# Performance work log

Measured on AMD Instinct MI355X. Metric: run time of the kernel, lower is better.

The kernel has to match this reference:

```python
import jax, jax.numpy as jnp
import numpy as np

B, T, D_IN, H, BR, D_OUT = 256, 500, 700, 200, 2, 35
V_TH = 1.0


def setup_inputs() -> dict:
    key = jax.random.key(0)
    ks = jax.random.split(key, 7)
    x = jax.random.normal(ks[0], (B, T, D_IN), dtype=jnp.float32)
    W_in = jax.random.normal(ks[1], (H * BR, D_IN), dtype=jnp.float32) * (1.0 / np.sqrt(D_IN))
    b_in = jax.random.normal(ks[2], (H * BR,), dtype=jnp.float32) * 0.01
    # tau_n ~ U(0, 4) per branch per neuron (as in SimpleDH_LIF init)
    tau_n = jax.random.uniform(ks[3], (H, BR), dtype=jnp.float32, minval=0.0, maxval=4.0)
    tau_m = jnp.full((H,), 2.0, dtype=jnp.float32)  # torch init: tensor(2.0) per neuron
    W_out = jax.random.normal(ks[5], (D_OUT, H), dtype=jnp.float32) * (1.0 / np.sqrt(H))
    b_out = jax.random.normal(ks[6], (D_OUT,), dtype=jnp.float32) * 0.01
    return {"x": x, "W_in": W_in, "b_in": b_in, "tau_n": tau_n,
            "tau_m": tau_m, "W_out": W_out, "b_out": b_out}


def reference(x, W_in, b_in, tau_n, tau_m, W_out, b_out):
    b, t, _ = x.shape
    # Batched input projection for all timesteps at once: (B,T,H*BR) -> (T,B,H,BR)
    branch_in = jnp.einsum('bti,oi->bto', x, W_in) + b_in
    branch_in = branch_in.reshape(b, t, H, BR).transpose(1, 0, 2, 3)

    beta = jax.nn.sigmoid(tau_n)          # (H, BR) dendritic branch decay
    alpha = jax.nn.sigmoid(tau_m)         # (H,)   soma membrane decay

    def step(carry, inp_t):
        v, i_d, counts = carry            # v:(B,H) i_d:(B,H,BR) counts:(B,H)
        i_d = beta * i_d + (1.0 - beta) * inp_t
        i_total = i_d.sum(axis=-1)        # (B,H)
        v = alpha * v + (1.0 - alpha) * i_total
        spike = (v >= V_TH).astype(v.dtype)
        v = v - spike * V_TH
        return (v, i_d, counts + spike), None

    v0 = jnp.zeros((b, H), dtype=x.dtype)
    i0 = jnp.zeros((b, H, BR), dtype=x.dtype)
    c0 = jnp.zeros((b, H), dtype=x.dtype)
    (v, i_d, spike_counts), _ = jax.lax.scan(step, (v0, i0, c0), branch_in)

    return spike_counts @ W_out.T + b_out  # (B, D_OUT)
```

## Files before the change

kernel.cpp:

```cpp
#include <hip/hip_runtime.h>

#define B_   256
#define T_   500
#define DIN  700
#define KP   704
#define H_   200
#define NO   400
#define DOUT 35

typedef _Float16 half_t;
typedef __attribute__((ext_vector_type(8))) _Float16 half8;
typedef __attribute__((ext_vector_type(4))) float floatx4;

#define SX 16.0f
#define SW 4096.0f
#define INV_S (1.0f / 65536.0f)

__device__ __forceinline__ float sigmoidf_(float x) {
    return 1.0f / (1.0f + expf(-x));
}

__global__ __launch_bounds__(256) void cvt_split(
    const float* __restrict__ src, half_t* __restrict__ hi,
    half_t* __restrict__ lo, int rows, float scale)
{
    int idx = blockIdx.x * 256 + threadIdx.x;
    int row = idx / 176;
    int q   = idx - row * 176;
    if (row >= rows) return;
    float4 v = make_float4(0.f, 0.f, 0.f, 0.f);
    if (q < 175) v = *reinterpret_cast<const float4*>(&src[(size_t)row * DIN + q * 4]);
    float s0 = v.x * scale, s1 = v.y * scale, s2 = v.z * scale, s3 = v.w * scale;
    half_t h0 = (half_t)s0, h1 = (half_t)s1, h2 = (half_t)s2, h3 = (half_t)s3;
    half_t l0 = (half_t)(s0 - (float)h0);
    half_t l1 = (half_t)(s1 - (float)h1);
    half_t l2 = (half_t)(s2 - (float)h2);
    half_t l3 = (half_t)(s3 - (float)h3);
    size_t o = (size_t)row * KP + q * 4;
    half_t hv[4] = {h0, h1, h2, h3};
    half_t lv[4] = {l0, l1, l2, l3};
    *reinterpret_cast<ushort4*>(&hi[o]) = *reinterpret_cast<ushort4*>(hv);
    *reinterpret_cast<ushort4*>(&lo[o]) = *reinterpret_cast<ushort4*>(lv);
}

__global__ __launch_bounds__(256) void dh_gemm_fused(
    const float* __restrict__ x,
    const half_t* __restrict__ Wh, const half_t* __restrict__ Wl,
    const float* __restrict__ bin, float* __restrict__ Y)
{
    __shared__ half_t Ah[256][40], Al[256][40];
    __shared__ half_t Bh[80][40],  Bl[80][40];

    int p = blockIdx.x;
    int xcd = p & 7, slot = p >> 3;
    int L = (xcd < 4 ? xcd * 313 : 4 * 313 + (xcd - 4) * 312) + slot;
    int by = L / 5, bx = L - by * 5;
    const int m0 = by * 256, o0 = bx * 80;

    const int tid  = threadIdx.x;
    const int w    = tid >> 6;
    const int lane = tid & 63;
    const int la   = lane & 15;
    const int lb   = lane >> 4;

    const int srow = tid >> 2, sseg = tid & 3;
    const int brow = srow & 63;

    floatx4 acc[4][5];
    #pragma unroll
    for (int mf = 0; mf < 4; ++mf)
        #pragma unroll
        for (int nf = 0; nf < 5; ++nf) {
            floatx4 z = {0.f, 0.f, 0.f, 0.f};
            acc[mf][nf] = z;
        }

    float4 rAf[4][2];
    half8 rBh[2], rBl[2];

    auto LOAD = [&](int kc) {
        const int k0 = kc * 32;
        const int kcol = k0 + sseg * 8;
        #pragma unroll
        for (int i = 0; i < 4; ++i) {
            const float* src = &x[(size_t)(m0 + srow + i * 64) * DIN + kcol];
            rAf[i][0] = *reinterpret_cast<const float4*>(src);
            if (kcol + 8 <= DIN)
                rAf[i][1] = *reinterpret_cast<const float4*>(src + 4);
            else
                rAf[i][1] = make_float4(0.f, 0.f, 0.f, 0.f);
        }
        if (tid < 160) {
            #pragma unroll
            for (int i = 0; i < 2; ++i) {
                size_t g = (size_t)(o0 + brow + i * 40) * KP + k0 + sseg * 8;
                rBh[i] = *reinterpret_cast<const half8*>(&Wh[g]);
                rBl[i] = *reinterpret_cast<const half8*>(&Wl[g]);
            }
        }
    };

    LOAD(0);

    for (int kc = 0; kc < 22; ++kc) {
        __syncthreads();
        #pragma unroll
        for (int i = 0; i < 4; ++i) {
            float vv[8];
            *reinterpret_cast<float4*>(&vv[0]) = rAf[i][0];
            *reinterpret_cast<float4*>(&vv[4]) = rAf[i][1];
            half8 hh, ll;
            #pragma unroll
            for (int j = 0; j < 8; ++j) {
                float s = vv[j] * SX;
                half_t h = (half_t)s;
                hh[j] = h;
                ll[j] = (half_t)(s - (float)h);
            }
            *reinterpret_cast<half8*>(&Ah[srow + i * 64][sseg * 8]) = hh;
            *reinterpret_cast<half8*>(&Al[srow + i * 64][sseg * 8]) = ll;
        }
        if (tid < 160) {
            #pragma unroll
            for (int i = 0; i < 2; ++i) {
                *reinterpret_cast<half8*>(&Bh[brow + i * 40][sseg * 8]) = rBh[i];
                *reinterpret_cast<half8*>(&Bl[brow + i * 40][sseg * 8]) = rBl[i];
            }
        }
        __syncthreads();

        if (kc + 1 < 22) LOAD(kc + 1);

        half8 ah[4], al[4], bh[5], bl[5];
        #pragma unroll
        for (int mf = 0; mf < 4; ++mf) {
            int r = w * 64 + mf * 16 + la;
            ah[mf] = *reinterpret_cast<const half8*>(&Ah[r][lb * 8]);
            al[mf] = *reinterpret_cast<const half8*>(&Al[r][lb * 8]);
        }
        #pragma unroll
        for (int nf = 0; nf < 5; ++nf) {
            int r = nf * 16 + la;
            bh[nf] = *reinterpret_cast<const half8*>(&Bh[r][lb * 8]);
            bl[nf] = *reinterpret_cast<const half8*>(&Bl[r][lb * 8]);
        }
        #pragma unroll
        for (int mf = 0; mf < 4; ++mf)
            #pragma unroll
            for (int nf = 0; nf < 5; ++nf)
                acc[mf][nf] = __builtin_amdgcn_mfma_f32_16x16x32_f16(ah[mf], bh[nf], acc[mf][nf], 0, 0, 0);
        #pragma unroll
        for (int mf = 0; mf < 4; ++mf)
            #pragma unroll
            for (int nf = 0; nf < 5; ++nf)
                acc[mf][nf] = __builtin_amdgcn_mfma_f32_16x16x32_f16(ah[mf], bl[nf], acc[mf][nf], 0, 0, 0);
        #pragma unroll
        for (int mf = 0; mf < 4; ++mf)
            #pragma unroll
            for (int nf = 0; nf < 5; ++nf)
                acc[mf][nf] = __builtin_amdgcn_mfma_f32_16x16x32_f16(al[mf], bh[nf], acc[mf][nf], 0, 0, 0);
    }

    float bo[5];
    #pragma unroll
    for (int nf = 0; nf < 5; ++nf) bo[nf] = bin[o0 + nf * 16 + la];

    #pragma unroll
    for (int mf = 0; mf < 4; ++mf) {
        int mbase = m0 + w * 64 + mf * 16 + lb * 4;
        #pragma unroll
        for (int rg = 0; rg < 4; ++rg) {
            int mm = mbase + rg;
            int bb = mm / T_;
            int tt = mm - bb * T_;
            float* yrow = &Y[((size_t)tt * B_ + bb) * NO + o0 + la];
            #pragma unroll
            for (int nf = 0; nf < 5; ++nf)
                yrow[nf * 16] = acc[mf][nf][rg] * INV_S + bo[nf];
        }
    }
}

#define BM 256
#define BN 64
#define BK 16
__global__ __launch_bounds__(256) void dh_gemm_in(
    const float* __restrict__ x, const float* __restrict__ Wt,
    const float* __restrict__ bin, float* __restrict__ Y)
{
    __shared__ float As[BK][BM + 4];
    __shared__ float Bs[BK][BN + 4];
    const int tid = threadIdx.x;
    const int tx = tid & 7;
    const int ty = tid >> 3;
    const int m0 = blockIdx.y * BM;
    const int o0 = blockIdx.x * BN;

    float acc[8][8];
    #pragma unroll
    for (int r = 0; r < 8; ++r)
        #pragma unroll
        for (int c = 0; c < 8; ++c) acc[r][c] = 0.0f;

    const int srow = tid >> 2;
    const int skq  = (tid & 3) << 2;

    for (int k0 = 0; k0 < DIN; k0 += BK) {
        float4 areg[4];
        #pragma unroll
        for (int i = 0; i < 4; ++i) {
            int idx = tid + i * 256;
            int row = idx >> 2;
            int kq  = (idx & 3) << 2;
            int kg  = k0 + kq;
            if (kg < DIN)
                areg[i] = *reinterpret_cast<const float4*>(&x[(size_t)(m0 + row) * DIN + kg]);
            else
                areg[i] = make_float4(0.f, 0.f, 0.f, 0.f);
        }
        float4 breg;
        {
            int kg = k0 + skq;
            int o  = o0 + srow;
            if (kg < DIN && o < NO)
                breg = *reinterpret_cast<const float4*>(&Wt[(size_t)o * DIN + kg]);
            else
                breg = make_float4(0.f, 0.f, 0.f, 0.f);
        }
        __syncthreads();
        #pragma unroll
        for (int i = 0; i < 4; ++i) {
            int idx = tid + i * 256;
            int row = idx >> 2;
            int kq  = (idx & 3) << 2;
            As[kq + 0][row] = areg[i].x;
            As[kq + 1][row] = areg[i].y;
            As[kq + 2][row] = areg[i].z;
            As[kq + 3][row] = areg[i].w;
        }
        Bs[skq + 0][srow] = breg.x;
        Bs[skq + 1][srow] = breg.y;
        Bs[skq + 2][srow] = breg.z;
        Bs[skq + 3][srow] = breg.w;
        __syncthreads();

        #pragma unroll
        for (int k = 0; k < BK; ++k) {
            float a[8], bb[8];
            *reinterpret_cast<float4*>(&a[0])  = *reinterpret_cast<const float4*>(&As[k][ty * 8]);
            *reinterpret_cast<float4*>(&a[4])  = *reinterpret_cast<const float4*>(&As[k][ty * 8 + 4]);
            *reinterpret_cast<float4*>(&bb[0]) = *reinterpret_cast<const float4*>(&Bs[k][tx * 8]);
            *reinterpret_cast<float4*>(&bb[4]) = *reinterpret_cast<const float4*>(&Bs[k][tx * 8 + 4]);
            #pragma unroll
            for (int r = 0; r < 8; ++r)
                #pragma unroll
                for (int c = 0; c < 8; ++c)
                    acc[r][c] = fmaf(a[r], bb[c], acc[r][c]);
        }
    }

    float bo[8];
    #pragma unroll
    for (int c = 0; c < 8; ++c) {
        int o = o0 + tx * 8 + c;
        bo[c] = (o < NO) ? bin[o] : 0.0f;
    }
    const int ob = o0 + tx * 8;
    if (ob < NO) {
        #pragma unroll
        for (int r = 0; r < 8; ++r) {
            int m = m0 + ty * 8 + r;
            int b = m / T_;
            int t = m - b * T_;
            float* yrow = &Y[((size_t)t * B_ + b) * NO];
            float4 v0 = make_float4(acc[r][0] + bo[0], acc[r][1] + bo[1],
                                    acc[r][2] + bo[2], acc[r][3] + bo[3]);
            float4 v1 = make_float4(acc[r][4] + bo[4], acc[r][5] + bo[5],
                                    acc[r][6] + bo[6], acc[r][7] + bo[7]);
            *reinterpret_cast<float4*>(&yrow[ob])     = v0;
            *reinterpret_cast<float4*>(&yrow[ob + 4]) = v1;
        }
    }
}

__global__ __launch_bounds__(64) void dh_scan(
    const float* __restrict__ Y, const float* __restrict__ tau_n,
    const float* __restrict__ tau_m, float* __restrict__ counts)
{
    int g = blockIdx.x * 64 + threadIdx.x;
    int b = g / H_;
    int h = g - b * H_;
    (void)b;
    float beta0 = sigmoidf_(tau_n[h * 2 + 0]);
    float beta1 = sigmoidf_(tau_n[h * 2 + 1]);
    float alpha = sigmoidf_(tau_m[h]);
    float omb0 = 1.0f - beta0, omb1 = 1.0f - beta1, oma = 1.0f - alpha;
    const float2* Yp = reinterpret_cast<const float2*>(Y);

    float v = 0.f, i0 = 0.f, i1 = 0.f, cnt = 0.f;
    #pragma unroll 1
    for (int t0 = 0; t0 < T_; t0 += 10) {
        float2 yb[10];
        #pragma unroll
        for (int j = 0; j < 10; ++j)
            yb[j] = Yp[(size_t)(t0 + j) * (B_ * H_) + g];
        #pragma unroll
        for (int j = 0; j < 10; ++j) {
            i0 = beta0 * i0 + omb0 * yb[j].x;
            i1 = beta1 * i1 + omb1 * yb[j].y;
            float it = i0 + i1;
            v = alpha * v + oma * it;
            if (v >= 1.0f) { v -= 1.0f; cnt += 1.0f; }
        }
    }
    counts[g] = cnt;
}

__global__ __launch_bounds__(64) void dh_out(
    const float* __restrict__ counts, const float* __restrict__ W_out,
    const float* __restrict__ b_out, float* __restrict__ out)
{
    int b = blockIdx.x;
    int o = threadIdx.x;
    if (o >= DOUT) return;
    float acc = b_out[o];
    const float* c = &counts[(size_t)b * H_];
    const float* w = &W_out[(size_t)o * H_];
    #pragma unroll 4
    for (int h = 0; h < H_; ++h)
        acc = fmaf(c[h], w[h], acc);
    out[(size_t)b * DOUT + o] = acc;
}

extern "C" void kernel_launch(void* const* d_in, const int* in_sizes, int n_in,
                              void* d_out, int out_size, void* d_ws, size_t ws_size,
                              hipStream_t stream) {
    const float* x     = (const float*)d_in[0];
    const float* W_in  = (const float*)d_in[1];
    const float* b_in  = (const float*)d_in[2];
    const float* tau_n = (const float*)d_in[3];
    const float* tau_m = (const float*)d_in[4];
    const float* W_out = (const float*)d_in[5];
    const float* b_out = (const float*)d_in[6];
    float* out = (float*)d_out;

    float* Y      = (float*)d_ws;
    float* counts = Y + (size_t)T_ * B_ * NO;

    size_t need_f16 = (size_t)T_ * B_ * NO * 4 + (size_t)B_ * H_ * 4
                    + 2 * ((size_t)NO * KP * 2);

    if (ws_size >= need_f16) {
        half_t* Wh = (half_t*)(counts + (size_t)B_ * H_);
        half_t* Wl = Wh + (size_t)NO * KP;

        cvt_split<<<(NO * 176 + 255) / 256, 256, 0, stream>>>(W_in, Wh, Wl, NO, SW);
        dh_gemm_fused<<<2500, 256, 0, stream>>>(x, Wh, Wl, b_in, Y);
    } else {
        dim3 g1(7, 500);
        dh_gemm_in<<<g1, 256, 0, stream>>>(x, W_in, b_in, Y);
    }

    dh_scan<<<(B_ * H_) / 64, 64, 0, stream>>>(Y, tau_n, tau_m, counts);
    dh_out<<<B_, 64, 0, stream>>>(counts, W_out, b_out, out);
}
```

Before: 424.7 us.

## Drop LDS staging in input GEMM; pre-swizzle W into MFMA fragment layout

Replaces the LDS-staged block GEMM with a per-wave kernel that loads x directly from global memory into MFMA fragment registers. W_in's hi/lo f16 split is stored in fragment order so each lane does contiguous loads. Loads are double-buffered in registers across pairs of K-chunks, and all __syncthreads and shared-memory traffic are removed. In exchange, wave tiles no longer share A/B data through LDS, which raises global/L2 traffic and register pressure (launch_bounds 256,2).

```diff
diff --git a/kernel.cpp b/kernel.cpp
--- a/kernel.cpp
+++ b/kernel.cpp
@@ -7,6 +7,7 @@
 #define H_   200
 #define NO   400
 #define DOUT 35
+#define NKC  22
 
 typedef _Float16 half_t;
 typedef __attribute__((ext_vector_type(8))) _Float16 half8;
@@ -20,51 +21,49 @@
     return 1.0f / (1.0f + expf(-x));
 }
 
-__global__ __launch_bounds__(256) void cvt_split(
-    const float* __restrict__ src, half_t* __restrict__ hi,
-    half_t* __restrict__ lo, int rows, float scale)
-{
-    int idx = blockIdx.x * 256 + threadIdx.x;
-    int row = idx / 176;
-    int q   = idx - row * 176;
-    if (row >= rows) return;
-    float4 v = make_float4(0.f, 0.f, 0.f, 0.f);
-    if (q < 175) v = *reinterpret_cast<const float4*>(&src[(size_t)row * DIN + q * 4]);
-    float s0 = v.x * scale, s1 = v.y * scale, s2 = v.z * scale, s3 = v.w * scale;
-    half_t h0 = (half_t)s0, h1 = (half_t)s1, h2 = (half_t)s2, h3 = (half_t)s3;
-    half_t l0 = (half_t)(s0 - (float)h0);
-    half_t l1 = (half_t)(s1 - (float)h1);
-    half_t l2 = (half_t)(s2 - (float)h2);
-    half_t l3 = (half_t)(s3 - (float)h3);
-    size_t o = (size_t)row * KP + q * 4;
-    half_t hv[4] = {h0, h1, h2, h3};
-    half_t lv[4] = {l0, l1, l2, l3};
-    *reinterpret_cast<ushort4*>(&hi[o]) = *reinterpret_cast<ushort4*>(hv);
-    *reinterpret_cast<ushort4*>(&lo[o]) = *reinterpret_cast<ushort4*>(lv);
-}
-
-__global__ __launch_bounds__(256) void dh_gemm_fused(
+__global__ __launch_bounds__(256) void cvt_wfrag(
+    const float* __restrict__ W, half_t* __restrict__ Whf, half_t* __restrict__ Wlf)
+{
+    int t = blockIdx.x * 256 + threadIdx.x;
+    if (t >= NKC * 25 * 64) return;
+    int lane = t & 63;
+    int rest = t >> 6;
+    int nfg  = rest % 25;
+    int kc   = rest / 25;
+    int la = lane & 15, lb = lane >> 4;
+    int row = nfg * 16 + la;
+    int col = kc * 32 + lb * 8;
+    half8 hh, ll;
+    #pragma unroll
+    for (int j = 0; j < 8; ++j) {
+        float v = (col + j < DIN) ? W[(size_t)row * DIN + col + j] : 0.0f;
+        float s = v * SW;
+        half_t h = (half_t)s;
+        hh[j] = h;
+        ll[j] = (half_t)(s - (float)h);
+    }
+    *reinterpret_cast<half8*>(&Whf[(size_t)t * 8]) = hh;
+    *reinterpret_cast<half8*>(&Wlf[(size_t)t * 8]) = ll;
+}
+
+__global__ __launch_bounds__(256, 2) void dh_gemm_nolds(
     const float* __restrict__ x,
-    const half_t* __restrict__ Wh, const half_t* __restrict__ Wl,
+    const half_t* __restrict__ Whf, const half_t* __restrict__ Wlf,
     const float* __restrict__ bin, float* __restrict__ Y)
 {
-    __shared__ half_t Ah[256][40], Al[256][40];
-    __shared__ half_t Bh[80][40],  Bl[80][40];
-
     int p = blockIdx.x;
     int xcd = p & 7, slot = p >> 3;
     int L = (xcd < 4 ? xcd * 313 : 4 * 313 + (xcd - 4) * 312) + slot;
-    int by = L / 5, bx = L - by * 5;
-    const int m0 = by * 256, o0 = bx * 80;
-
-    const int tid  = threadIdx.x;
-    const int w    = tid >> 6;
-    const int lane = tid & 63;
+
+    const int w    = threadIdx.x >> 6;
+    const int lane = threadIdx.x & 63;
     const int la   = lane & 15;
     const int lb   = lane >> 4;
 
-    const int srow = tid >> 2, sseg = tid & 3;
-    const int brow = srow & 63;
+    const int wave = L * 4 + w;
+    const int mt = wave / 5, nt = wave - mt * 5;
+    const int m0 = mt * 64;
+    const int o0 = nt * 80;
 
     floatx4 acc[4][5];
     #pragma unroll
@@ -75,40 +74,41 @@
             acc[mf][nf] = z;
         }
 
-    float4 rAf[4][2];
-    half8 rBh[2], rBl[2];
-
-    auto LOAD = [&](int kc) {
-        const int k0 = kc * 32;
-        const int kcol = k0 + sseg * 8;
-        #pragma unroll
-        for (int i = 0; i < 4; ++i) {
-            const float* src = &x[(size_t)(m0 + srow + i * 64) * DIN + kcol];
-            rAf[i][0] = *reinterpret_cast<const float4*>(src);
-            if (kcol + 8 <= DIN)
-                rAf[i][1] = *reinterpret_cast<const float4*>(src + 4);
-            else
-                rAf[i][1] = make_float4(0.f, 0.f, 0.f, 0.f);
-        }
-        if (tid < 160) {
-            #pragma unroll
-            for (int i = 0; i < 2; ++i) {
-                size_t g = (size_t)(o0 + brow + i * 40) * KP + k0 + sseg * 8;
-                rBh[i] = *reinterpret_cast<const half8*>(&Wh[g]);
-                rBl[i] = *reinterpret_cast<const half8*>(&Wl[g]);
-            }
+    size_t arow[4];
+    #pragma unroll
+    for (int mf = 0; mf < 4; ++mf)
+        arow[mf] = (size_t)(m0 + mf * 16 + la) * DIN;
+    const size_t bbase = ((size_t)(nt * 5) * 64 + lane) * 8;
+
+    float4 ra0[4][2], ra1[4][2];
+    half8 b0h[5], b0l[5], b1h[5], b1l[5];
+    half8 ah[4], al[4];
+
+    auto LOADA = [&](float4 (&ra)[4][2], int kc) {
+        const int col = kc * 32 + lb * 8;
+        const int c2ofs = (col + 8 <= DIN) ? 4 : (692 - col);
+        #pragma unroll
+        for (int mf = 0; mf < 4; ++mf) {
+            const float* ptr = &x[arow[mf] + col];
+            ra[mf][0] = *reinterpret_cast<const float4*>(ptr);
+            ra[mf][1] = *reinterpret_cast<const float4*>(ptr + c2ofs);
         }
     };
-
-    LOAD(0);
-
-    for (int kc = 0; kc < 22; ++kc) {
-        __syncthreads();
-        #pragma unroll
-        for (int i = 0; i < 4; ++i) {
+    auto LOADB = [&](half8 (&bh)[5], half8 (&bl)[5], int kc) {
+        const size_t kofs = (size_t)kc * 25 * 64 * 8;
+        #pragma unroll
+        for (int nf = 0; nf < 5; ++nf) {
+            size_t idx = bbase + kofs + (size_t)nf * 64 * 8;
+            bh[nf] = *reinterpret_cast<const half8*>(&Whf[idx]);
+            bl[nf] = *reinterpret_cast<const half8*>(&Wlf[idx]);
+        }
+    };
+    auto CONV = [&](const float4 (&ra)[4][2]) {
+        #pragma unroll
+        for (int mf = 0; mf < 4; ++mf) {
             float vv[8];
-            *reinterpret_cast<float4*>(&vv[0]) = rAf[i][0];
-            *reinterpret_cast<float4*>(&vv[4]) = rAf[i][1];
+            *reinterpret_cast<float4*>(&vv[0]) = ra[mf][0];
+            *reinterpret_cast<float4*>(&vv[4]) = ra[mf][1];
             half8 hh, ll;
             #pragma unroll
             for (int j = 0; j < 8; ++j) {
@@ -117,33 +117,11 @@
                 hh[j] = h;
                 ll[j] = (half_t)(s - (float)h);
             }
-            *reinterpret_cast<half8*>(&Ah[srow + i * 64][sseg * 8]) = hh;
-            *reinterpret_cast<half8*>(&Al[srow + i * 64][sseg * 8]) = ll;
-        }
-        if (tid < 160) {
-            #pragma unroll
-            for (int i = 0; i < 2; ++i) {
-                *reinterpret_cast<half8*>(&Bh[brow + i * 40][sseg * 8]) = rBh[i];
-                *reinterpret_cast<half8*>(&Bl[brow + i * 40][sseg * 8]) = rBl[i];
-            }
-        }
-        __syncthreads();
-
-        if (kc + 1 < 22) LOAD(kc + 1);
-
-        half8 ah[4], al[4], bh[5], bl[5];
-        #pragma unroll
-        for (int mf = 0; mf < 4; ++mf) {
-            int r = w * 64 + mf * 16 + la;
-            ah[mf] = *reinterpret_cast<const half8*>(&Ah[r][lb * 8]);
-            al[mf] = *reinterpret_cast<const half8*>(&Al[r][lb * 8]);
-        }
-        #pragma unroll
-        for (int nf = 0; nf < 5; ++nf) {
-            int r = nf * 16 + la;
-            bh[nf] = *reinterpret_cast<const half8*>(&Bh[r][lb * 8]);
-            bl[nf] = *reinterpret_cast<const half8*>(&Bl[r][lb * 8]);
-        }
+            ah[mf] = hh;
+            al[mf] = ll;
+        }
+    };
+    auto MFMAS = [&](const half8 (&bh)[5], const half8 (&bl)[5]) {
         #pragma unroll
         for (int mf = 0; mf < 4; ++mf)
             #pragma unroll
@@ -159,6 +137,22 @@
             #pragma unroll
             for (int nf = 0; nf < 5; ++nf)
                 acc[mf][nf] = __builtin_amdgcn_mfma_f32_16x16x32_f16(al[mf], bh[nf], acc[mf][nf], 0, 0, 0);
+    };
+
+    LOADA(ra0, 0);
+    LOADB(b0h, b0l, 0);
+    #pragma unroll 1
+    for (int kc2 = 0; kc2 < NKC; kc2 += 2) {
+        LOADA(ra1, kc2 + 1);
+        LOADB(b1h, b1l, kc2 + 1);
+        CONV(ra0);
+        MFMAS(b0h, b0l);
+        if (kc2 + 2 < NKC) {
+            LOADA(ra0, kc2 + 2);
+            LOADB(b0h, b0l, kc2 + 2);
+        }
+        CONV(ra1);
+        MFMAS(b1h, b1l);
     }
 
     float bo[5];
@@ -167,7 +161,7 @@
 
     #pragma unroll
     for (int mf = 0; mf < 4; ++mf) {
-        int mbase = m0 + w * 64 + mf * 16 + lb * 4;
+        int mbase = m0 + mf * 16 + lb * 4;
         #pragma unroll
         for (int rg = 0; rg < 4; ++rg) {
             int mm = mbase + rg;
@@ -347,15 +341,16 @@
     float* Y      = (float*)d_ws;
     float* counts = Y + (size_t)T_ * B_ * NO;
 
-    size_t need_f16 = (size_t)T_ * B_ * NO * 4 + (size_t)B_ * H_ * 4
-                    + 2 * ((size_t)NO * KP * 2);
-
-    if (ws_size >= need_f16) {
-        half_t* Wh = (half_t*)(counts + (size_t)B_ * H_);
-        half_t* Wl = Wh + (size_t)NO * KP;
-
-        cvt_split<<<(NO * 176 + 255) / 256, 256, 0, stream>>>(W_in, Wh, Wl, NO, SW);
-        dh_gemm_fused<<<2500, 256, 0, stream>>>(x, Wh, Wl, b_in, Y);
+    const size_t nfrag_halves = (size_t)NKC * 25 * 64 * 8;
+    size_t need = ((size_t)T_ * B_ * NO + (size_t)B_ * H_) * 4
+                + 2 * nfrag_halves * 2;
+
+    if (ws_size >= need) {
+        half_t* Whf = (half_t*)(counts + (size_t)B_ * H_);
+        half_t* Wlf = Whf + nfrag_halves;
+
+        cvt_wfrag<<<(NKC * 25 * 64 + 255) / 256, 256, 0, stream>>>(W_in, Whf, Wlf);
+        dh_gemm_nolds<<<2500, 256, 0, stream>>>(x, Whf, Wlf, b_in, Y);
     } else {
         dim3 g1(7, 500);
         dh_gemm_in<<<g1, 256, 0, stream>>>(x, W_in, b_in, Y);
```

After: 413.1 us. 1.03x faster.
